# Performance work log

Hardware: AMD Instinct MI355X
Metric: run time of the kernel (lower is better)

The kernel has to match this reference:

```python
import jax, jax.numpy as jnp
import numpy as np

K = 3          # kernel_size
STRIDE = 1
PAD = 1
NUM_BASIS = 8
DEGREE = 3
M = NUM_BASIS + DEGREE   # number of basis slots (11)
EPS = 1e-5               # BatchNorm2d default eps


def _unfold(x):
    # x: [B,C,H,W] -> patches [B,C,L,K*K] (L = Ho*Wo spatial positions, last dim = kernel pos)
    x = jnp.pad(x, ((0, 0), (0, 0), (PAD, PAD), (PAD, PAD)))
    B, C, H, W = x.shape
    Ho = (H - K) // STRIDE + 1
    Wo = (W - K) // STRIDE + 1
    ii = (jnp.arange(Ho) * STRIDE)[:, None] + jnp.arange(K)[None, :]   # [Ho,K]
    jj = (jnp.arange(Wo) * STRIDE)[:, None] + jnp.arange(K)[None, :]   # [Wo,K]
    p = x[:, :, ii[:, None, :, None], jj[None, :, None, :]]           # [B,C,Ho,Wo,K,K]
    return p.reshape(B, C, Ho * Wo, K * K), Ho, Wo


def _bspline_basis(u):
    # Vectorized Cox-de Boor recursion, faithful to the module's in-place update
    # (entries j >= M-d keep their stale lower-degree values, as in the original).
    # u: [...,] in (0,1) -> basis [..., M]
    knots = jnp.linspace(0.0, 1.0, M + 1).astype(u.dtype)              # 12 knots
    b = ((u[..., None] >= knots[:M]) & (u[..., None] < knots[1:M + 1])).astype(u.dtype)
    for d in range(1, DEGREE + 1):
        n = M - d
        j = np.arange(n)
        den1 = knots[j + d] - knots[j]
        den2 = knots[j + d + 1] - knots[j + 1]
        alpha = jnp.where(den1 != 0, (u[..., None] - knots[j]) / jnp.where(den1 != 0, den1, 1.0), 0.0)
        beta = jnp.where(den2 != 0, (knots[j + d + 1] - u[..., None]) / jnp.where(den2 != 0, den2, 1.0), 0.0)
        upd = alpha * b[..., :n] + beta * b[..., 1:n + 1]
        b = jnp.concatenate([upd, b[..., n:]], axis=-1)
    return b


def setup_inputs() -> dict:
    key = jax.random.key(0)
    k1, k2, k3 = jax.random.split(key, 3)
    B, C_in, C_out, H, W = 8, 64, 128, 56, 56
    x = jax.random.normal(k1, (B, C_in, H, W), dtype=jnp.float32)
    # Xavier-uniform-like scale for control points [O, C, K*K, M]
    fan = C_in * K * K * M + C_out
    bound_cp = float(np.sqrt(6.0 / fan))
    control_points = jax.random.uniform(k2, (C_out, C_in, K * K, M), minval=-bound_cp, maxval=bound_cp, dtype=jnp.float32)
    bound_w = float(np.sqrt(6.0 / (C_in * K * K + C_out * K * K)))
    conv_w = jax.random.uniform(k3, (C_out, C_in, K, K), minval=-bound_w, maxval=bound_w, dtype=jnp.float32)
    conv_b = jnp.zeros((C_out,), dtype=jnp.float32)
    bn_gamma = jnp.ones((C_out,), dtype=jnp.float32)
    bn_beta = jnp.zeros((C_out,), dtype=jnp.float32)
    return {"x": x, "control_points": control_points, "conv_w": conv_w,
            "conv_b": conv_b, "bn_gamma": bn_gamma, "bn_beta": bn_beta}


def reference(x, control_points, conv_w, conv_b, bn_gamma, bn_beta):
    patches, Ho, Wo = _unfold(x)                 # [B,C,L,K2]
    u = jax.nn.sigmoid(patches)
    basis = _bspline_basis(u)                    # [B,C,L,K2,M]
    # spline output: contract in_channels, kernel positions, basis index
    spline = jnp.einsum('bclkn,ockn->bol', basis, control_points)
    B = x.shape[0]
    O = control_points.shape[0]
    spline = spline.reshape(B, O, Ho, Wo)
    conv = jax.lax.conv_general_dilated(x, conv_w, (STRIDE, STRIDE), [(PAD, PAD), (PAD, PAD)],
                                        dimension_numbers=('NCHW', 'OIHW', 'NCHW'))
    out = spline + conv + conv_b[None, :, None, None]
    # Dropout2d is identity in eval mode. BatchNorm2d with batch statistics (training default).
    mean = out.mean(axis=(0, 2, 3), keepdims=True)
    var = out.var(axis=(0, 2, 3), keepdims=True)
    out = (out - mean) * jax.lax.rsqrt(var + EPS)
    return out * bn_gamma[None, :, None, None] + bn_beta[None, :, None, None]
```

## Files before the change

### kernel.cpp

```cpp
#include <hip/hip_runtime.h>
#include <math.h>

#define CIN   64
#define COUT  128
#define HW    56
#define L_    3136
#define KTOT  6912
#define TH    8
#define TW    8
#define HALO_W 10
#define NPIX  100
#define CSTR  (NPIX*16)
#define G8_SIZE (8*CSTR)
#define G4_SIZE (4*CSTR)
#define BUF_SIZE (G8_SIZE+G4_SIZE)

#define BP_BYTES (COUT * KTOT * 2)
#define PART_OFF BP_BYTES
#define SS_OFF   (PART_OFF + 2048 * 4)

typedef __attribute__((ext_vector_type(8))) short bf16x8;
typedef __attribute__((ext_vector_type(4))) float f32x4;
typedef unsigned long long u64;

#define BLOAD(dst, addr) \
    asm volatile("global_load_dwordx4 %0, %1, off" : "=v"(dst) : "v"(addr))
#define XLOAD(dst, addr) \
    asm volatile("global_load_dword %0, %1, off" : "=v"(dst) : "v"(addr))

__device__ __forceinline__ unsigned short f2bf(float f) {
    unsigned int u = __float_as_uint(f);
    return (unsigned short)((u + 0x7FFFu + ((u >> 16) & 1u)) >> 16);
}
__device__ __forceinline__ unsigned int pk2(float a, float b) {
    return (unsigned int)f2bf(a) | ((unsigned int)f2bf(b) << 16);
}

__device__ __forceinline__ void eval_store(float xv, char* g8rec, char* g4half) {
    float u  = 1.0f / (1.0f + __expf(-xv));
    float tt = u * 11.0f;
    int s = (int)floorf(tt);
    s = (s > 10) ? 10 : s;
    float xf  = tt - (float)s;
    float x2  = xf * xf, x3 = x2 * xf;
    float omx = 1.0f - xf;
    const float i6 = 1.0f / 6.0f;
    float w3 = x3 * i6;
    float w2 = fmaf(fmaf(fmaf(-3.0f, xf, 3.0f), xf, 3.0f), xf, 1.0f) * i6;
    float w1 = fmaf(fmaf(3.0f, xf, -6.0f), x2, 4.0f) * i6;
    float w0 = omx * omx * omx * i6;

    *reinterpret_cast<uint4*>(g8rec) = (uint4){0u, 0u, 0u, 0u};
    unsigned short* rec = reinterpret_cast<unsigned short*>(g8rec);
    {
        int j;
        j = s - 3; if (j >= 0 && j < 8) rec[j] = f2bf(w0);
        j = s - 2; if (j >= 0 && j < 8) rec[j] = f2bf(w1);
        j = s - 1; if (j >= 0 && j < 8) rec[j] = f2bf(w2);
        j = s;     if (j >= 0 && j < 8) rec[j] = f2bf(w3);
    }
    float y = tt - 8.0f;
    float f8 = 0.0f;
    f8 = (s == 8)  ? 0.5f * y * y : f8;
    f8 = (s == 9)  ? 0.5f * fmaf(-2.0f * y, y, fmaf(6.0f, y, -3.0f)) : f8;
    f8 = (s == 10) ? 0.5f * (3.0f - y) * (3.0f - y) : f8;
    float z = tt - 9.0f;
    float f9 = 0.0f;
    f9 = (s == 9)  ? z : f9;
    f9 = (s == 10) ? 2.0f - z : f9;
    float f10 = (s == 10) ? 1.0f : 0.0f;
    *reinterpret_cast<uint2*>(g4half) = make_uint2(pk2(f8, f9), pk2(f10, xv));
}

__global__ __launch_bounds__(256) void k_packB(const float* __restrict__ cp,
                                               const float* __restrict__ w,
                                               unsigned short* __restrict__ Bp) {
    int idx = blockIdx.x * 256 + threadIdx.x;
    if (idx >= COUT * KTOT) return;
    int kstep = idx >> 12;
    int rem   = idx & 4095;
    int o     = rem >> 5;
    int e32   = rem & 31;
    int ch = kstep / 27, sc = kstep - ch * 27;
    int ktap = sc / 3, ph = sc - ktap * 3;
    int c, n;
    if (ph < 2) { c = ch * 8 + ph * 4 + (e32 >> 3); n = e32 & 7; }
    else        { int sub = e32 & 7; c = ch * 8 + (e32 >> 3) * 2 + (sub >> 2); n = 8 + (sub & 3); }
    float v;
    if (n < 11) v = cp[(((size_t)o * CIN + c) * 9 + ktap) * 11 + n];
    else        v = w[((size_t)o * CIN + c) * 9 + ktap];
    Bp[idx] = f2bf(v);
}

__global__ __launch_bounds__(256, 2) void k_main(const float* __restrict__ x,
                                                 const unsigned short* __restrict__ Bp,
                                                 const float* __restrict__ bias,
                                                 float* __restrict__ out) {
    __shared__ char lds[2 * BUF_SIZE];

    const int bid  = blockIdx.x;
    const int b    = bid / 49;
    const int tile = bid - b * 49;
    const int th   = tile / 7;
    const int tw   = tile - th * 7;
    const int t    = threadIdx.x;
    const int lane = t & 63;
    const int wid  = t >> 6;

    const bool valid = (t < 200);
    const int p    = (t < 100) ? t : (t - 100);
    const int hi100 = (t >= 100) ? 1 : 0;
    const int ph_  = p / 10, pw_ = p - ph_ * 10;
    const int hg = th * TH - 1 + ph_;
    const int wg = tw * TW - 1 + pw_;
    const bool inb = valid && (hg >= 0) && (hg < HW) && (wg >= 0) && (wg < HW);
    const u64 xadv = inb ? (u64)8 * L_ * 4 : 0;
    u64 px[4];
#pragma unroll
    for (int r = 0; r < 4; r++) {
        int c0 = 2 * r + hi100;
        px[r] = inb ? ((u64)x + (((u64)b * CIN + c0) * L_ + (u64)hg * HW + wg) * 4)
                    : (u64)x;
    }

    const int q   = lane >> 4;
    const int r15 = lane & 15;
    int P[4];
#pragma unroll
    for (int mi = 0; mi < 4; mi++) {
        int lh = mi * 2 + (r15 >> 3);
        int lw = r15 & 7;
        P[mi] = (lh * HALO_W + lw) * 16 + q * CSTR;
    }
    const int obase = wid * 32 + r15;

    const u64 bend = (u64)Bp + BP_BYTES;
    u64 pa0 = (u64)Bp + ((u64)obase * 64) + ((u64)q * 16);
    u64 pa1 = pa0 + 1024;

    f32x4 acc[4][2];
#pragma unroll
    for (int mi = 0; mi < 4; mi++)
#pragma unroll
        for (int ni = 0; ni < 2; ni++) acc[mi][ni] = (f32x4){0.f, 0.f, 0.f, 0.f};

    float xa[4];
    XLOAD(xa[0], px[0]); XLOAD(xa[1], px[1]);
    XLOAD(xa[2], px[2]); XLOAD(xa[3], px[3]);
#pragma unroll
    for (int r = 0; r < 4; r++) px[r] += xadv;
    asm volatile("s_waitcnt vmcnt(0)");
    __builtin_amdgcn_sched_barrier(0);
    if (valid) {
#pragma unroll
        for (int r = 0; r < 4; r++) {
            float va = inb ? xa[r] : 0.0f;
            int c = 2 * r + hi100;
            eval_store(va, &lds[c * CSTR + p * 16],
                       &lds[G8_SIZE + r * CSTR + p * 16 + hi100 * 8]);
        }
    }
    asm volatile("s_waitcnt lgkmcnt(0)");
    __builtin_amdgcn_s_barrier();

    bf16x8 breg0[9], breg1[9];
#pragma unroll
    for (int s = 0; s < 9; s++) {
        BLOAD(breg0[s], pa0);
        BLOAD(breg1[s], pa1);
        pa0 += 8192; pa1 += 8192;
    }

#pragma unroll 1
    for (int ch = 0; ch < 8; ch++) {
        XLOAD(xa[0], px[0]); XLOAD(xa[1], px[1]);
        XLOAD(xa[2], px[2]); XLOAD(xa[3], px[3]);
        if (ch < 7) {
#pragma unroll
            for (int r = 0; r < 4; r++) px[r] += xadv;
        }

        char* abuf = &lds[(ch & 1) * BUF_SIZE];
        char* nbuf = &lds[((ch + 1) & 1) * BUF_SIZE];

        bf16x8 areg[2][4];
        auto aread = [&](int s, bf16x8 (&a)[4]) {
            int k = s / 3, bp = s - k * 3;
            int ki = k / 3, kj = k - ki * 3;
            int poff = (ki * HALO_W + kj) * 16;
            int aoff = (bp == 2) ? (G8_SIZE + poff) : (bp * 4 * CSTR + poff);
#pragma unroll
            for (int mi = 0; mi < 4; mi++)
                a[mi] = *reinterpret_cast<const bf16x8*>(abuf + P[mi] + aoff);
        };
        aread(0, areg[0]);

#pragma unroll
        for (int s = 0; s < 27; s++) {
            if (s + 1 < 27) aread(s + 1, areg[(s + 1) & 1]);
            asm volatile("s_waitcnt vmcnt(16)");
            __builtin_amdgcn_sched_barrier(0);
            const int bs = s % 9;
#pragma unroll
            for (int mi = 0; mi < 4; mi++) {
                acc[mi][0] = __builtin_amdgcn_mfma_f32_16x16x32_bf16(areg[s & 1][mi], breg0[bs], acc[mi][0], 0, 0, 0);
                acc[mi][1] = __builtin_amdgcn_mfma_f32_16x16x32_bf16(areg[s & 1][mi], breg1[bs], acc[mi][1], 0, 0, 0);
            }
            BLOAD(breg0[bs], pa0);
            BLOAD(breg1[bs], pa1);
            pa0 += 8192; if (pa0 >= bend) pa0 -= BP_BYTES;
            pa1 += 8192; if (pa1 >= bend) pa1 -= BP_BYTES;
        }

        if (ch < 7 && valid) {
#pragma unroll
            for (int r = 0; r < 4; r++) {
                float va = inb ? xa[r] : 0.0f;
                int c = 2 * r + hi100;
                eval_store(va, &nbuf[c * CSTR + p * 16],
                           &nbuf[G8_SIZE + r * CSTR + p * 16 + hi100 * 8]);
            }
        }
        asm volatile("s_waitcnt lgkmcnt(0)");
        __builtin_amdgcn_s_barrier();
    }

    asm volatile("s_waitcnt vmcnt(0)");

#pragma unroll
    for (int ni = 0; ni < 2; ni++) {
        int o = obase + ni * 16;
        float bv = bias[o];
#pragma unroll
        for (int mi = 0; mi < 4; mi++) {
            int lh = mi * 2 + (q >> 1);
            int lw0 = (q & 1) * 4;
            int lg = (th * TH + lh) * HW + tw * TW + lw0;
            float4 v;
            v.x = acc[mi][ni][0] + bv;
            v.y = acc[mi][ni][1] + bv;
            v.z = acc[mi][ni][2] + bv;
            v.w = acc[mi][ni][3] + bv;
            *reinterpret_cast<float4*>(&out[(size_t)(b * COUT + o) * L_ + lg]) = v;
        }
    }
}

__global__ __launch_bounds__(256) void k_part(const float* __restrict__ s,
                                              float* __restrict__ part) {
    const int slab = blockIdx.x;
    const float4* p4 = reinterpret_cast<const float4*>(s + (size_t)slab * L_);
    const int t = threadIdx.x;
    float sum = 0.f, sq = 0.f;
    for (int i = t; i < L_ / 4; i += 256) {
        float4 v = p4[i];
        sum += v.x + v.y + v.z + v.w;
        sq  += v.x * v.x + v.y * v.y + v.z * v.z + v.w * v.w;
    }
    __shared__ float rs[256], rq[256];
    rs[t] = sum; rq[t] = sq;
    __syncthreads();
    for (int off = 128; off > 0; off >>= 1) {
        if (t < off) { rs[t] += rs[t + off]; rq[t] += rq[t + off]; }
        __syncthreads();
    }
    if (t == 0) { part[slab] = rs[0]; part[1024 + slab] = rq[0]; }
}

__global__ __launch_bounds__(128) void k_final(const float* __restrict__ part,
                                               const float* __restrict__ gamma,
                                               const float* __restrict__ beta,
                                               float* __restrict__ ss) {
    int o = threadIdx.x;
    float sum = 0.f, sq = 0.f;
#pragma unroll
    for (int b = 0; b < 8; b++) {
        sum += part[b * COUT + o];
        sq  += part[1024 + b * COUT + o];
    }
    float n = (float)(8 * L_);
    float mean = sum / n;
    float var  = sq / n - mean * mean;
    float scale = gamma[o] * rsqrtf(var + 1e-5f);
    ss[o]        = scale;
    ss[COUT + o] = beta[o] - mean * scale;
}

__global__ __launch_bounds__(256) void k_norm(float* __restrict__ out,
                                              const float* __restrict__ ss) {
    const int n4 = 8 * COUT * L_ / 4;
    for (int i = blockIdx.x * 256 + threadIdx.x; i < n4; i += gridDim.x * 256) {
        int o = ((i * 4) / L_) & (COUT - 1);
        float sc = ss[o], sh = ss[COUT + o];
        float4 v = reinterpret_cast<float4*>(out)[i];
        v.x = fmaf(v.x, sc, sh);
        v.y = fmaf(v.y, sc, sh);
        v.z = fmaf(v.z, sc, sh);
        v.w = fmaf(v.w, sc, sh);
        reinterpret_cast<float4*>(out)[i] = v;
    }
}

extern "C" void kernel_launch(void* const* d_in, const int* in_sizes, int n_in,
                              void* d_out, int out_size, void* d_ws, size_t ws_size,
                              hipStream_t stream) {
    const float* x     = (const float*)d_in[0];
    const float* cp    = (const float*)d_in[1];
    const float* w     = (const float*)d_in[2];
    const float* bias  = (const float*)d_in[3];
    const float* gamma = (const float*)d_in[4];
    const float* beta  = (const float*)d_in[5];
    float* out = (float*)d_out;

    unsigned short* Bp = (unsigned short*)d_ws;
    float* part = (float*)((char*)d_ws + PART_OFF);
    float* ss   = (float*)((char*)d_ws + SS_OFF);

    k_packB<<<(COUT * KTOT + 255) / 256, 256, 0, stream>>>(cp, w, Bp);
    k_main<<<8 * 49, 256, 0, stream>>>(x, Bp, bias, out);
    k_part<<<1024, 256, 0, stream>>>(out, part);
    k_final<<<1, 128, 0, stream>>>(part, gamma, beta, ss);
    k_norm<<<2048, 256, 0, stream>>>(out, ss);
}
```

Measured before the change: 86.81 us.

## Split K dimension across two blocks per tile with atomic accumulation

Splits the input-channel reduction of the main GEMM into two halves, doubling the grid from 392 to 784 blocks so more CUs have work on a 256-CU device. Each block accumulates its half and adds the result into the output with float atomics. A new pre-pass kernel initializes the output with the bias. This costs an extra full-output write pass plus atomic read-modify-write traffic, and makes the summation order nondeterministic.

```diff
diff --git a/kernel.cpp b/kernel.cpp
--- a/kernel.cpp
+++ b/kernel.cpp
@@ -92,15 +92,26 @@
     Bp[idx] = f2bf(v);
 }
 
+__global__ __launch_bounds__(256) void k_bias(float* __restrict__ out,
+                                              const float* __restrict__ bias) {
+    const int n4 = 8 * COUT * L_ / 4;
+    for (int i = blockIdx.x * 256 + threadIdx.x; i < n4; i += gridDim.x * 256) {
+        int o = ((i * 4) / L_) & (COUT - 1);
+        float bv = bias[o];
+        reinterpret_cast<float4*>(out)[i] = (float4){bv, bv, bv, bv};
+    }
+}
+
 __global__ __launch_bounds__(256, 2) void k_main(const float* __restrict__ x,
                                                  const unsigned short* __restrict__ Bp,
-                                                 const float* __restrict__ bias,
                                                  float* __restrict__ out) {
     __shared__ char lds[2 * BUF_SIZE];
 
     const int bid  = blockIdx.x;
-    const int b    = bid / 49;
-    const int tile = bid - b * 49;
+    const int kh   = bid & 1;
+    const int tb   = bid >> 1;
+    const int b    = tb / 49;
+    const int tile = tb - b * 49;
     const int th   = tile / 7;
     const int tw   = tile - th * 7;
     const int t    = threadIdx.x;
@@ -108,7 +119,7 @@
     const int wid  = t >> 6;
 
     const bool valid = (t < 200);
-    const int p    = (t < 100) ? t : (t - 100);
+    const int p     = (t < 100) ? t : (t - 100);
     const int hi100 = (t >= 100) ? 1 : 0;
     const int ph_  = p / 10, pw_ = p - ph_ * 10;
     const int hg = th * TH - 1 + ph_;
@@ -118,7 +129,7 @@
     u64 px[4];
 #pragma unroll
     for (int r = 0; r < 4; r++) {
-        int c0 = 2 * r + hi100;
+        int c0 = kh * 32 + 2 * r + hi100;
         px[r] = inb ? ((u64)x + (((u64)b * CIN + c0) * L_ + (u64)hg * HW + wg) * 4)
                     : (u64)x;
     }
@@ -135,7 +146,7 @@
     const int obase = wid * 32 + r15;
 
     const u64 bend = (u64)Bp + BP_BYTES;
-    u64 pa0 = (u64)Bp + ((u64)obase * 64) + ((u64)q * 16);
+    u64 pa0 = (u64)Bp + (u64)kh * 108 * 8192 + ((u64)obase * 64) + ((u64)q * 16);
     u64 pa1 = pa0 + 1024;
 
     f32x4 acc[4][2];
@@ -160,8 +171,7 @@
                        &lds[G8_SIZE + r * CSTR + p * 16 + hi100 * 8]);
         }
     }
-    asm volatile("s_waitcnt lgkmcnt(0)");
-    __builtin_amdgcn_s_barrier();
+    __syncthreads();
 
     bf16x8 breg0[9], breg1[9];
 #pragma unroll
@@ -172,16 +182,16 @@
     }
 
 #pragma unroll 1
-    for (int ch = 0; ch < 8; ch++) {
+    for (int cr = 0; cr < 4; cr++) {
         XLOAD(xa[0], px[0]); XLOAD(xa[1], px[1]);
         XLOAD(xa[2], px[2]); XLOAD(xa[3], px[3]);
-        if (ch < 7) {
+        if (cr < 2) {
 #pragma unroll
             for (int r = 0; r < 4; r++) px[r] += xadv;
         }
 
-        char* abuf = &lds[(ch & 1) * BUF_SIZE];
-        char* nbuf = &lds[((ch + 1) & 1) * BUF_SIZE];
+        char* abuf = &lds[(cr & 1) * BUF_SIZE];
+        char* nbuf = &lds[((cr + 1) & 1) * BUF_SIZE];
 
         bf16x8 areg[2][4];
         auto aread = [&](int s, bf16x8 (&a)[4]) {
@@ -212,7 +222,7 @@
             pa1 += 8192; if (pa1 >= bend) pa1 -= BP_BYTES;
         }
 
-        if (ch < 7 && valid) {
+        if (cr < 3 && valid) {
 #pragma unroll
             for (int r = 0; r < 4; r++) {
                 float va = inb ? xa[r] : 0.0f;
@@ -221,27 +231,24 @@
                            &nbuf[G8_SIZE + r * CSTR + p * 16 + hi100 * 8]);
             }
         }
-        asm volatile("s_waitcnt lgkmcnt(0)");
-        __builtin_amdgcn_s_barrier();
+        __syncthreads();
     }
 
     asm volatile("s_waitcnt vmcnt(0)");
+    __builtin_amdgcn_sched_barrier(0);
 
 #pragma unroll
     for (int ni = 0; ni < 2; ni++) {
         int o = obase + ni * 16;
-        float bv = bias[o];
 #pragma unroll
         for (int mi = 0; mi < 4; mi++) {
             int lh = mi * 2 + (q >> 1);
             int lw0 = (q & 1) * 4;
             int lg = (th * TH + lh) * HW + tw * TW + lw0;
-            float4 v;
-            v.x = acc[mi][ni][0] + bv;
-            v.y = acc[mi][ni][1] + bv;
-            v.z = acc[mi][ni][2] + bv;
-            v.w = acc[mi][ni][3] + bv;
-            *reinterpret_cast<float4*>(&out[(size_t)(b * COUT + o) * L_ + lg]) = v;
+            float* pdst = &out[(size_t)(b * COUT + o) * L_ + lg];
+#pragma unroll
+            for (int j = 0; j < 4; j++)
+                atomicAdd(pdst + j, acc[mi][ni][j]);
         }
     }
 }
@@ -317,7 +324,8 @@
     float* ss   = (float*)((char*)d_ws + SS_OFF);
 
     k_packB<<<(COUT * KTOT + 255) / 256, 256, 0, stream>>>(cp, w, Bp);
-    k_main<<<8 * 49, 256, 0, stream>>>(x, Bp, bias, out);
+    k_bias<<<2048, 256, 0, stream>>>(out, bias);
+    k_main<<<784, 256, 0, stream>>>(x, Bp, out);
     k_part<<<1024, 256, 0, stream>>>(out, part);
     k_final<<<1, 128, 0, stream>>>(part, gamma, beta, ss);
     k_norm<<<2048, 256, 0, stream>>>(out, ss);
```

New measurement: 228.5 us. +163.2%, slower.
